# Kernel optimization log

Measured on AMD Instinct MI355X. Metric: run time of the kernel, lower is better.

Reference implementation:

```python
import jax, jax.numpy as jnp
import numpy as np

HIDDEN = 1024
HEADS = 16
B, L = 2, 2048


def _xavier(key, shape):
    fan_in, fan_out = shape[1], shape[0]
    limit = float(np.sqrt(6.0 / (fan_in + fan_out)))
    return jax.random.uniform(key, shape, jnp.float32, -limit, limit)


def setup_inputs() -> dict:
    key = jax.random.key(0)
    ks = jax.random.split(key, 6)
    return {
        "query": jax.random.normal(ks[0], (B, L, HIDDEN), jnp.float32),
        "bias": jax.random.normal(ks[1], (B, 1, 1, L), jnp.float32),
        "Wq": _xavier(ks[2], (HIDDEN, HIDDEN)), "bq": jnp.zeros((HIDDEN,), jnp.float32),
        "Wk": _xavier(ks[3], (HIDDEN, HIDDEN)), "bk": jnp.zeros((HIDDEN,), jnp.float32),
        "Wv": _xavier(ks[4], (HIDDEN, HIDDEN)), "bv": jnp.zeros((HIDDEN,), jnp.float32),
        "Wo": _xavier(ks[5], (HIDDEN, HIDDEN)), "bo": jnp.zeros((HIDDEN,), jnp.float32),
    }


def _split_heads(x):
    b, l, c = x.shape
    return x.reshape(b, l, HEADS, c // HEADS).transpose(0, 2, 1, 3)  # [B,H,L,d]


def reference(query, bias, Wq, bq, Wk, bk, Wv, bv, Wo, bo):
    d_head = HIDDEN // HEADS
    q = query @ Wq.T + bq
    k = query @ Wk.T + bk
    v = query @ Wv.T + bv
    q = _split_heads(q) * (d_head ** -0.5)  # [B,H,L,d]
    k = _split_heads(k)
    v = _split_heads(v)
    logits = jnp.einsum("bhqd,bhkd->bhqk", q, k) + bias  # [B,H,L,L]
    weights = jax.nn.softmax(logits, axis=-1)
    x = jnp.einsum("bhqk,bhkd->bhqd", weights, v)  # [B,H,L,d]
    x = x.transpose(0, 2, 1, 3).reshape(query.shape[0], query.shape[1], HIDDEN)
    return x @ Wo.T + bo
```

## Files before the change

kernel.cpp:

```cpp
#include <hip/hip_runtime.h>
#include <hip/hip_fp16.h>
#include <stdint.h>

#define HIDDEN 1024
#define HEADS  16
#define DH     64
#define B_     2
#define L_     2048
#define M_TOT  (B_ * L_)
#define ELEMS  (M_TOT * HIDDEN)
#define LOG2E  1.44269504088896340736f

typedef _Float16 f16;
typedef _Float16 f16x4 __attribute__((ext_vector_type(4)));
typedef _Float16 f16x8 __attribute__((ext_vector_type(8)));
typedef float    f32x4 __attribute__((ext_vector_type(4)));
typedef uint32_t u32;
typedef __attribute__((address_space(1))) u32 gu32;
typedef __attribute__((address_space(3))) u32 su32;

#define MFMA16(a, b, c) __builtin_amdgcn_mfma_f32_16x16x16f16(a, b, c, 0, 0, 0)
#define MFMA32(a, b, c) __builtin_amdgcn_mfma_f32_16x16x32_f16(a, b, c, 0, 0, 0)


__global__ __launch_bounds__(256)
void convert_f16(const float* __restrict__ query,
                 const float* __restrict__ Wq, const float* __restrict__ Wk,
                 const float* __restrict__ Wv, const float* __restrict__ Wo,
                 f16* __restrict__ Qh, f16* __restrict__ Wh)
{
    const int NQ4 = ELEMS / 4;
    const int NW4 = (HIDDEN * HIDDEN) / 4;
    const int total = NQ4 + 4 * NW4;
    for (int u = blockIdx.x * 256 + threadIdx.x; u < total; u += gridDim.x * 256) {
        float4 v; f16* dp;
        if (u < NQ4) {
            v = ((const float4*)query)[u];
            dp = Qh + (size_t)u * 4;
        } else {
            const int u2 = u - NQ4;
            const int w = u2 >> 18;
            const int off = u2 & (NW4 - 1);
            const float* W = (w == 0) ? Wq : (w == 1) ? Wk : (w == 2) ? Wv : Wo;
            v = ((const float4*)W)[off];
            dp = Wh + (size_t)u2 * 4;
        }
        f16x4 h = { (f16)v.x, (f16)v.y, (f16)v.z, (f16)v.w };
        *(f16x4*)dp = h;
    }
}

template<int TM, int TN>
__device__ __forceinline__
void gemm_loop(const f16* __restrict__ A, const f16* __restrict__ W,
               int mb, int nb, f32x4 (&acc)[TM / 32][TN / 32])
{
    __shared__ f16 As[TM * 32];
    __shared__ f16 Bs[TN * 32];

    const int tid  = threadIdx.x;
    const int lane = tid & 63;
    const int wave = tid >> 6;
    const int quad = lane >> 4;
    const int l16  = lane & 15;
    const int wm   = (wave >> 1) * (TM / 2);
    const int wn   = (wave & 1) * (TN / 2);

    constexpr int AISS = TM / 64;
    constexpr int BISS = TN / 64;
    int aoff[AISS], boff[BISS];
#pragma unroll
    for (int q = 0; q < AISS; q++) {
        const int p16 = (wave * AISS + q) * 64 + lane;
        const int r = p16 >> 2;
        const int c8 = (p16 & 3) ^ ((r >> 1) & 3);
        aoff[q] = (mb + r) * HIDDEN + c8 * 8;
    }
#pragma unroll
    for (int q = 0; q < BISS; q++) {
        const int p16 = (wave * BISS + q) * 64 + lane;
        const int r = p16 >> 2;
        const int c8 = (p16 & 3) ^ ((r >> 1) & 3);
        boff[q] = (nb + r) * HIDDEN + c8 * 8;
    }

    for (int kb = 0; kb < HIDDEN; kb += 32) {
#pragma unroll
        for (int q = 0; q < AISS; q++)
            __builtin_amdgcn_global_load_lds((gu32*)&A[aoff[q] + kb],
                                             (su32*)&As[(wave * AISS + q) * 512], 16, 0, 0);
#pragma unroll
        for (int q = 0; q < BISS; q++)
            __builtin_amdgcn_global_load_lds((gu32*)&W[boff[q] + kb],
                                             (su32*)&Bs[(wave * BISS + q) * 512], 16, 0, 0);
        __syncthreads();

        f16x8 af[TM / 32], bf[TN / 32];
#pragma unroll
        for (int i = 0; i < TM / 32; i++) {
            const int r = wm + i * 16 + l16;
            af[i] = *(const f16x8*)&As[r * 32 + (quad ^ ((r >> 1) & 3)) * 8];
        }
#pragma unroll
        for (int j = 0; j < TN / 32; j++) {
            const int r = wn + j * 16 + l16;
            bf[j] = *(const f16x8*)&Bs[r * 32 + (quad ^ ((r >> 1) & 3)) * 8];
        }
#pragma unroll
        for (int i = 0; i < TM / 32; i++)
#pragma unroll
            for (int j = 0; j < TN / 32; j++)
                acc[i][j] = MFMA32(af[i], bf[j], acc[i][j]);
        __syncthreads();
    }
}

__global__ __launch_bounds__(256)
void proj_qkv(const f16* __restrict__ A, const f16* __restrict__ W,
              const float* __restrict__ bq, const float* __restrict__ bk,
              const float* __restrict__ bv,
              f16* __restrict__ Qo, f16* __restrict__ Ko, f16* __restrict__ Vo)
{
    f32x4 acc[4][4] = {};
    const int mb = blockIdx.x * 128, nb = blockIdx.y * 128;
    gemm_loop<128, 128>(A, W, mb, nb, acc);

    const int lane = threadIdx.x & 63, wave = threadIdx.x >> 6;
    const int quad = lane >> 4, l16 = lane & 15;
    const int wm = (wave >> 1) * 64, wn = (wave & 1) * 64;
    const int nsel = nb >> 10;
    const int nbase = nb & 1023;

    if (nsel < 2) {
        const float* bias = nsel ? bk : bq;
        f16* out = nsel ? Ko : Qo;
        const float scale = nsel ? 1.0f : 0.125f * LOG2E;
#pragma unroll
        for (int i = 0; i < 4; i++)
#pragma unroll
            for (int j = 0; j < 4; j++) {
                const int n1 = nbase + wn + j * 16 + l16;
                const float bn = bias[n1];
                const int h = n1 >> 6, dd = n1 & 63;
#pragma unroll
                for (int r = 0; r < 4; r++) {
                    const int m = mb + wm + i * 16 + quad * 4 + r;
                    const int b = m >> 11, l = m & (L_ - 1);
                    out[(((b * HEADS + h) * L_) + l) * DH + dd] =
                        (f16)((acc[i][j][r] + bn) * scale);
                }
            }
    } else {
#pragma unroll
        for (int i = 0; i < 4; i++)
#pragma unroll
            for (int j = 0; j < 4; j++) {
                const int n1 = nbase + wn + j * 16 + l16;
                const float bn = bv[n1];
                const int h = n1 >> 6, dd = n1 & 63;
                const int m0 = mb + wm + i * 16 + quad * 4;
                const int b = m0 >> 11, l0 = m0 & (L_ - 1);
                f16x4 pk;
#pragma unroll
                for (int r = 0; r < 4; r++) pk[r] = (f16)(acc[i][j][r] + bn);
                *(f16x4*)&Vo[((size_t)(b * HEADS + h) * DH + dd) * L_ + l0] = pk;
            }
    }
}

__global__ __launch_bounds__(256)
void proj_out(const f16* __restrict__ A, const f16* __restrict__ W,
              const float* __restrict__ bo, float* __restrict__ out)
{
    f32x4 acc[4][2] = {};
    const int mb = blockIdx.x * 128, nb = blockIdx.y * 64;
    gemm_loop<128, 64>(A, W, mb, nb, acc);

    const int lane = threadIdx.x & 63, wave = threadIdx.x >> 6;
    const int quad = lane >> 4, l16 = lane & 15;
    const int wm = (wave >> 1) * 64, wn = (wave & 1) * 32;
#pragma unroll
    for (int i = 0; i < 4; i++)
#pragma unroll
        for (int j = 0; j < 2; j++) {
            const int n = nb + wn + j * 16 + l16;
            const float bn = bo[n];
#pragma unroll
            for (int r = 0; r < 4; r++) {
                const int m = mb + wm + i * 16 + quad * 4 + r;
                out[m * HIDDEN + n] = acc[i][j][r] + bn;
            }
        }
}

__global__ __launch_bounds__(256)
void attn(const f16* __restrict__ Q, const f16* __restrict__ K,
          const f16* __restrict__ Vt, const float* __restrict__ bias,
          f16* __restrict__ X)
{
    __shared__ f16 Ks[2][64 * 64];
    __shared__ f16 Vs[2][64 * 64];
    __shared__ float biasl[L_];

    const int tid  = threadIdx.x;
    const int lane = tid & 63;
    const int wave = tid >> 6;
    const int quad = lane >> 4;
    const int l16  = lane & 15;

    const int bh = blockIdx.x >> 4;
    const int b  = bh >> 4, h = bh & 15;
    const int qrow0 = (blockIdx.x & 15) * 128 + wave * 32;

    const f16* Qh  = Q  + (size_t)bh * L_ * DH;
    const f16* Kh  = K  + (size_t)bh * L_ * DH;
    const f16* Vth = Vt + (size_t)bh * DH * L_;

    {
        const float4* bb = (const float4*)(bias + b * L_);
        for (int i = tid; i < L_ / 4; i += 256) {
            const float4 v = bb[i];
            biasl[i * 4 + 0] = v.x * LOG2E;
            biasl[i * 4 + 1] = v.y * LOG2E;
            biasl[i * 4 + 2] = v.z * LOG2E;
            biasl[i * 4 + 3] = v.w * LOG2E;
        }
    }

    int krow[2], kcol[2];
#pragma unroll
    for (int q = 0; q < 2; q++) {
        const int grp = wave * 2 + q;
        const int r = grp * 8 + (lane >> 3);
        const int u = (lane & 7) ^ (r & 7);
        krow[q] = r; kcol[q] = u * 8;
    }

    f16x8 qf[2][2];
#pragma unroll
    for (int qt = 0; qt < 2; qt++)
#pragma unroll
        for (int hh = 0; hh < 2; hh++)
            qf[qt][hh] = *(const f16x8*)&Qh[(qrow0 + qt * 16 + l16) * DH + hh * 32 + quad * 8];

#pragma unroll
    for (int q = 0; q < 2; q++) {
        __builtin_amdgcn_global_load_lds((gu32*)(Kh + (size_t)krow[q] * DH + kcol[q]),
                                         (su32*)&Ks[0][(wave * 2 + q) * 512], 16, 0, 0);
        __builtin_amdgcn_global_load_lds((gu32*)(Vth + (size_t)krow[q] * L_ + kcol[q]),
                                         (su32*)&Vs[0][(wave * 2 + q) * 512], 16, 0, 0);
    }

    f32x4 o[2][4] = {};
    float lsum[2] = {};
    __syncthreads();

#pragma unroll 1
    for (int kb = 0; kb < L_; kb += 64) {
        const int buf = (kb >> 6) & 1;
        const int nkb = (kb + 64 < L_) ? kb + 64 : 0;

#pragma unroll
        for (int q = 0; q < 2; q++) {
            __builtin_amdgcn_global_load_lds(
                (gu32*)(Kh + (size_t)(nkb + krow[q]) * DH + kcol[q]),
                (su32*)&Ks[buf ^ 1][(wave * 2 + q) * 512], 16, 0, 0);
            __builtin_amdgcn_global_load_lds(
                (gu32*)(Vth + (size_t)krow[q] * L_ + nkb + kcol[q]),
                (su32*)&Vs[buf ^ 1][(wave * 2 + q) * 512], 16, 0, 0);
        }

#pragma unroll
        for (int c = 0; c < 4; c++) {
            const int krowc = c * 16 + l16;
            const f16x8 ka0 = *(const f16x8*)&Ks[buf][krowc * 64 + (quad ^ (krowc & 7)) * 8];
            const f16x8 ka1 = *(const f16x8*)&Ks[buf][krowc * 64 + ((quad + 4) ^ (krowc & 7)) * 8];
            f16x4 va[4];
#pragma unroll
            for (int t = 0; t < 4; t++) {
                const int vr = t * 16 + l16;
                const int uu = (c * 2 + (quad >> 1)) ^ (vr & 7);
                va[t] = *(const f16x4*)&Vs[buf][vr * 64 + uu * 8 + (quad & 1) * 4];
            }
            const f32x4 blv = *(const f32x4*)&biasl[kb + c * 16 + quad * 4];

#pragma unroll
            for (int qt = 0; qt < 2; qt++) {
                f32x4 z = { 0.f, 0.f, 0.f, 0.f };
                z = MFMA32(ka0, qf[qt][0], z);
                z = MFMA32(ka1, qf[qt][1], z);
                float p0 = __builtin_amdgcn_exp2f(z[0] + blv[0]);
                float p1 = __builtin_amdgcn_exp2f(z[1] + blv[1]);
                float p2 = __builtin_amdgcn_exp2f(z[2] + blv[2]);
                float p3 = __builtin_amdgcn_exp2f(z[3] + blv[3]);
                lsum[qt] += (p0 + p1) + (p2 + p3);
                const f16x4 pb = { (f16)p0, (f16)p1, (f16)p2, (f16)p3 };
#pragma unroll
                for (int t = 0; t < 4; t++)
                    o[qt][t] = MFMA16(va[t], pb, o[qt][t]);
            }
        }
        __syncthreads();
    }

#pragma unroll
    for (int qt = 0; qt < 2; qt++) {
        lsum[qt] += __shfl_xor(lsum[qt], 16);
        lsum[qt] += __shfl_xor(lsum[qt], 32);
    }

#pragma unroll
    for (int qt = 0; qt < 2; qt++) {
        const float inv = 1.0f / lsum[qt];
        const size_t qrow = (size_t)b * L_ + qrow0 + qt * 16 + l16;
#pragma unroll
        for (int t = 0; t < 4; t++) {
            f16x4 pk;
#pragma unroll
            for (int r = 0; r < 4; r++) pk[r] = (f16)(o[qt][t][r] * inv);
            *(f16x4*)&X[qrow * HIDDEN + h * DH + t * 16 + quad * 4] = pk;
        }
    }
}

extern "C" void kernel_launch(void* const* d_in, const int* in_sizes, int n_in,
                              void* d_out, int out_size, void* d_ws, size_t ws_size,
                              hipStream_t stream)
{
    const float* query = (const float*)d_in[0];
    const float* bias  = (const float*)d_in[1];
    const float* Wq = (const float*)d_in[2]; const float* bq = (const float*)d_in[3];
    const float* Wk = (const float*)d_in[4]; const float* bk = (const float*)d_in[5];
    const float* Wv = (const float*)d_in[6]; const float* bv = (const float*)d_in[7];
    const float* Wo = (const float*)d_in[8]; const float* bo = (const float*)d_in[9];
    float* out = (float*)d_out;

    f16* Wh = (f16*)d_ws;
    f16* Qh = Wh + 4096 * 1024;
    f16* Kf = Qh + ELEMS;
    f16* Vf = Kf + ELEMS;
    f16* Qf = Vf + ELEMS;
    f16* Xf = Qh;

    convert_f16<<<2048, 256, 0, stream>>>(query, Wq, Wk, Wv, Wo, Qh, Wh);
    proj_qkv<<<dim3(32, 24), 256, 0, stream>>>(Qh, Wh, bq, bk, bv, Qf, Kf, Vf);
    attn<<<512, 256, 0, stream>>>(Qf, Kf, Vf, bias, Xf);
    proj_out<<<dim3(32, 16), 256, 0, stream>>>(Xf, Wh + 3072 * 1024, bo, out);
}
```

Before: 222.6 us.

## Double-buffer GEMM LDS tiles and widen attention blocks to 512 threads

The shared GEMM loop now double-buffers its A/B LDS tiles, prefetching the next K-slice while MFMAs run on the current one, so global loads overlap with compute. The attention kernel moves to 512-thread blocks covering 256 query rows, which halves the number of times each K/V tile and the bias row are staged per head. Each thread now issues one K and one V async load per iteration instead of two. Trade-offs are double the GEMM LDS footprint and larger attention blocks, which may reduce occupancy. The GEMM loop appears to keep only one __syncthreads per iteration and drops the barrier after the load, which could risk a read/write race on the buffers.

New measurement: 382.5 us. +71.9%, slower.

```diff
diff --git a/kernel.cpp b/kernel.cpp
--- a/kernel.cpp
+++ b/kernel.cpp
@@ -55,8 +55,8 @@
 void gemm_loop(const f16* __restrict__ A, const f16* __restrict__ W,
                int mb, int nb, f32x4 (&acc)[TM / 32][TN / 32])
 {
-    __shared__ f16 As[TM * 32];
-    __shared__ f16 Bs[TN * 32];
+    __shared__ f16 As[2][TM * 32];
+    __shared__ f16 Bs[2][TN * 32];
 
     const int tid  = threadIdx.x;
     const int lane = tid & 63;
@@ -84,27 +84,39 @@
         boff[q] = (nb + r) * HIDDEN + c8 * 8;
     }
 
+#pragma unroll
+    for (int q = 0; q < AISS; q++)
+        __builtin_amdgcn_global_load_lds((gu32*)&A[aoff[q]],
+                                         (su32*)&As[0][(wave * AISS + q) * 512], 16, 0, 0);
+#pragma unroll
+    for (int q = 0; q < BISS; q++)
+        __builtin_amdgcn_global_load_lds((gu32*)&W[boff[q]],
+                                         (su32*)&Bs[0][(wave * BISS + q) * 512], 16, 0, 0);
+    __syncthreads();
+
     for (int kb = 0; kb < HIDDEN; kb += 32) {
+        const int buf = (kb >> 5) & 1;
+        const int nkb = (kb + 32 < HIDDEN) ? kb + 32 : 0;
+
 #pragma unroll
         for (int q = 0; q < AISS; q++)
-            __builtin_amdgcn_global_load_lds((gu32*)&A[aoff[q] + kb],
-                                             (su32*)&As[(wave * AISS + q) * 512], 16, 0, 0);
+            __builtin_amdgcn_global_load_lds((gu32*)&A[aoff[q] + nkb],
+                                             (su32*)&As[buf ^ 1][(wave * AISS + q) * 512], 16, 0, 0);
 #pragma unroll
         for (int q = 0; q < BISS; q++)
-            __builtin_amdgcn_global_load_lds((gu32*)&W[boff[q] + kb],
-                                             (su32*)&Bs[(wave * BISS + q) * 512], 16, 0, 0);
-        __syncthreads();
+            __builtin_amdgcn_global_load_lds((gu32*)&W[boff[q] + nkb],
+                                             (su32*)&Bs[buf ^ 1][(wave * BISS + q) * 512], 16, 0, 0);
 
         f16x8 af[TM / 32], bf[TN / 32];
 #pragma unroll
         for (int i = 0; i < TM / 32; i++) {
             const int r = wm + i * 16 + l16;
-            af[i] = *(const f16x8*)&As[r * 32 + (quad ^ ((r >> 1) & 3)) * 8];
+            af[i] = *(const f16x8*)&As[buf][r * 32 + (quad ^ ((r >> 1) & 3)) * 8];
         }
 #pragma unroll
         for (int j = 0; j < TN / 32; j++) {
             const int r = wn + j * 16 + l16;
-            bf[j] = *(const f16x8*)&Bs[r * 32 + (quad ^ ((r >> 1) & 3)) * 8];
+            bf[j] = *(const f16x8*)&Bs[buf][r * 32 + (quad ^ ((r >> 1) & 3)) * 8];
         }
 #pragma unroll
         for (int i = 0; i < TM / 32; i++)
@@ -193,7 +205,7 @@
         }
 }
 
-__global__ __launch_bounds__(256)
+__global__ __launch_bounds__(512, 6)
 void attn(const f16* __restrict__ Q, const f16* __restrict__ K,
           const f16* __restrict__ Vt, const float* __restrict__ bias,
           f16* __restrict__ X)
@@ -208,33 +220,24 @@
     const int quad = lane >> 4;
     const int l16  = lane & 15;
 
-    const int bh = blockIdx.x >> 4;
+    const int bh = blockIdx.x >> 3;
     const int b  = bh >> 4, h = bh & 15;
-    const int qrow0 = (blockIdx.x & 15) * 128 + wave * 32;
+    const int qrow0 = (blockIdx.x & 7) * 256 + wave * 32;
 
     const f16* Qh  = Q  + (size_t)bh * L_ * DH;
     const f16* Kh  = K  + (size_t)bh * L_ * DH;
     const f16* Vth = Vt + (size_t)bh * DH * L_;
 
     {
-        const float4* bb = (const float4*)(bias + b * L_);
-        for (int i = tid; i < L_ / 4; i += 256) {
-            const float4 v = bb[i];
-            biasl[i * 4 + 0] = v.x * LOG2E;
-            biasl[i * 4 + 1] = v.y * LOG2E;
-            biasl[i * 4 + 2] = v.z * LOG2E;
-            biasl[i * 4 + 3] = v.w * LOG2E;
-        }
-    }
-
-    int krow[2], kcol[2];
-#pragma unroll
-    for (int q = 0; q < 2; q++) {
-        const int grp = wave * 2 + q;
-        const int r = grp * 8 + (lane >> 3);
-        const int u = (lane & 7) ^ (r & 7);
-        krow[q] = r; kcol[q] = u * 8;
-    }
+        const float4 v = ((const float4*)(bias + b * L_))[tid];
+        biasl[tid * 4 + 0] = v.x * LOG2E;
+        biasl[tid * 4 + 1] = v.y * LOG2E;
+        biasl[tid * 4 + 2] = v.z * LOG2E;
+        biasl[tid * 4 + 3] = v.w * LOG2E;
+    }
+
+    const int srow = tid >> 3;
+    const int scol = ((tid & 7) ^ (srow & 7)) * 8;
 
     f16x8 qf[2][2];
 #pragma unroll
@@ -243,13 +246,10 @@
         for (int hh = 0; hh < 2; hh++)
             qf[qt][hh] = *(const f16x8*)&Qh[(qrow0 + qt * 16 + l16) * DH + hh * 32 + quad * 8];
 
-#pragma unroll
-    for (int q = 0; q < 2; q++) {
-        __builtin_amdgcn_global_load_lds((gu32*)(Kh + (size_t)krow[q] * DH + kcol[q]),
-                                         (su32*)&Ks[0][(wave * 2 + q) * 512], 16, 0, 0);
-        __builtin_amdgcn_global_load_lds((gu32*)(Vth + (size_t)krow[q] * L_ + kcol[q]),
-                                         (su32*)&Vs[0][(wave * 2 + q) * 512], 16, 0, 0);
-    }
+    __builtin_amdgcn_global_load_lds((gu32*)(Kh + (size_t)srow * DH + scol),
+                                     (su32*)&Ks[0][wave * 512], 16, 0, 0);
+    __builtin_amdgcn_global_load_lds((gu32*)(Vth + (size_t)srow * L_ + scol),
+                                     (su32*)&Vs[0][wave * 512], 16, 0, 0);
 
     f32x4 o[2][4] = {};
     float lsum[2] = {};
@@ -260,15 +260,10 @@
         const int buf = (kb >> 6) & 1;
         const int nkb = (kb + 64 < L_) ? kb + 64 : 0;
 
-#pragma unroll
-        for (int q = 0; q < 2; q++) {
-            __builtin_amdgcn_global_load_lds(
-                (gu32*)(Kh + (size_t)(nkb + krow[q]) * DH + kcol[q]),
-                (su32*)&Ks[buf ^ 1][(wave * 2 + q) * 512], 16, 0, 0);
-            __builtin_amdgcn_global_load_lds(
-                (gu32*)(Vth + (size_t)krow[q] * L_ + nkb + kcol[q]),
-                (su32*)&Vs[buf ^ 1][(wave * 2 + q) * 512], 16, 0, 0);
-        }
+        __builtin_amdgcn_global_load_lds((gu32*)(Kh + (size_t)(nkb + srow) * DH + scol),
+                                         (su32*)&Ks[buf ^ 1][wave * 512], 16, 0, 0);
+        __builtin_amdgcn_global_load_lds((gu32*)(Vth + (size_t)srow * L_ + nkb + scol),
+                                         (su32*)&Vs[buf ^ 1][wave * 512], 16, 0, 0);
 
 #pragma unroll
         for (int c = 0; c < 4; c++) {
@@ -344,6 +339,6 @@
 
     convert_f16<<<2048, 256, 0, stream>>>(query, Wq, Wk, Wv, Wo, Qh, Wh);
     proj_qkv<<<dim3(32, 24), 256, 0, stream>>>(Qh, Wh, bq, bk, bv, Qf, Kf, Vf);
-    attn<<<512, 256, 0, stream>>>(Qf, Kf, Vf, bias, Xf);
+    attn<<<256, 512, 0, stream>>>(Qf, Kf, Vf, bias, Xf);
     proj_out<<<dim3(32, 16), 256, 0, stream>>>(Xf, Wh + 3072 * 1024, bo, out);
 }
```

## Double-buffer GEMM LDS tiles and fold softmax bias and row-sum into MFMAs

Applied to the files above, without the earlier changes.

The projection GEMM loop now uses two LDS buffers, prefetching the next K-slice while computing on the current one, and drops one of the two barriers per iteration. In attention, the bias is fed in as the MFMA accumulator's initial value, so no separate adds are needed. The softmax row-sum is computed by an extra MFMA against a vector of ones, which replaces the scalar adds and the cross-lane shuffles. This doubles GEMM LDS usage, and the single remaining barrier must still cover the hazard between reading one buffer and overwriting the other. The row-sum is now accumulated from fp16-rounded probabilities, which slightly changes numerics.

After: 207.1 us. 7.0% less time.

```diff
diff --git a/kernel.cpp b/kernel.cpp
--- a/kernel.cpp
+++ b/kernel.cpp
@@ -55,8 +55,8 @@
 void gemm_loop(const f16* __restrict__ A, const f16* __restrict__ W,
                int mb, int nb, f32x4 (&acc)[TM / 32][TN / 32])
 {
-    __shared__ f16 As[TM * 32];
-    __shared__ f16 Bs[TN * 32];
+    __shared__ f16 As[2][TM * 32];
+    __shared__ f16 Bs[2][TN * 32];
 
     const int tid  = threadIdx.x;
     const int lane = tid & 63;
@@ -84,27 +84,39 @@
         boff[q] = (nb + r) * HIDDEN + c8 * 8;
     }
 
+#pragma unroll
+    for (int q = 0; q < AISS; q++)
+        __builtin_amdgcn_global_load_lds((gu32*)&A[aoff[q]],
+                                         (su32*)&As[0][(wave * AISS + q) * 512], 16, 0, 0);
+#pragma unroll
+    for (int q = 0; q < BISS; q++)
+        __builtin_amdgcn_global_load_lds((gu32*)&W[boff[q]],
+                                         (su32*)&Bs[0][(wave * BISS + q) * 512], 16, 0, 0);
+    __syncthreads();
+
     for (int kb = 0; kb < HIDDEN; kb += 32) {
+        const int buf = (kb >> 5) & 1;
+        const int nkb = (kb + 32 < HIDDEN) ? kb + 32 : 0;
+
 #pragma unroll
         for (int q = 0; q < AISS; q++)
-            __builtin_amdgcn_global_load_lds((gu32*)&A[aoff[q] + kb],
-                                             (su32*)&As[(wave * AISS + q) * 512], 16, 0, 0);
+            __builtin_amdgcn_global_load_lds((gu32*)&A[aoff[q] + nkb],
+                                             (su32*)&As[buf ^ 1][(wave * AISS + q) * 512], 16, 0, 0);
 #pragma unroll
         for (int q = 0; q < BISS; q++)
-            __builtin_amdgcn_global_load_lds((gu32*)&W[boff[q] + kb],
-                                             (su32*)&Bs[(wave * BISS + q) * 512], 16, 0, 0);
-        __syncthreads();
+            __builtin_amdgcn_global_load_lds((gu32*)&W[boff[q] + nkb],
+                                             (su32*)&Bs[buf ^ 1][(wave * BISS + q) * 512], 16, 0, 0);
 
         f16x8 af[TM / 32], bf[TN / 32];
 #pragma unroll
         for (int i = 0; i < TM / 32; i++) {
             const int r = wm + i * 16 + l16;
-            af[i] = *(const f16x8*)&As[r * 32 + (quad ^ ((r >> 1) & 3)) * 8];
+            af[i] = *(const f16x8*)&As[buf][r * 32 + (quad ^ ((r >> 1) & 3)) * 8];
         }
 #pragma unroll
         for (int j = 0; j < TN / 32; j++) {
             const int r = wn + j * 16 + l16;
-            bf[j] = *(const f16x8*)&Bs[r * 32 + (quad ^ ((r >> 1) & 3)) * 8];
+            bf[j] = *(const f16x8*)&Bs[buf][r * 32 + (quad ^ ((r >> 1) & 3)) * 8];
         }
 #pragma unroll
         for (int i = 0; i < TM / 32; i++)
@@ -252,7 +264,8 @@
     }
 
     f32x4 o[2][4] = {};
-    float lsum[2] = {};
+    f32x4 osum[2] = {};
+    const f16x4 ones = { (f16)1.f, (f16)1.f, (f16)1.f, (f16)1.f };
     __syncthreads();
 
 #pragma unroll 1
@@ -286,18 +299,17 @@
 
 #pragma unroll
             for (int qt = 0; qt < 2; qt++) {
-                f32x4 z = { 0.f, 0.f, 0.f, 0.f };
+                f32x4 z = blv;
                 z = MFMA32(ka0, qf[qt][0], z);
                 z = MFMA32(ka1, qf[qt][1], z);
-                float p0 = __builtin_amdgcn_exp2f(z[0] + blv[0]);
-                float p1 = __builtin_amdgcn_exp2f(z[1] + blv[1]);
-                float p2 = __builtin_amdgcn_exp2f(z[2] + blv[2]);
-                float p3 = __builtin_amdgcn_exp2f(z[3] + blv[3]);
-                lsum[qt] += (p0 + p1) + (p2 + p3);
-                const f16x4 pb = { (f16)p0, (f16)p1, (f16)p2, (f16)p3 };
+                const f16x4 pb = { (f16)__builtin_amdgcn_exp2f(z[0]),
+                                   (f16)__builtin_amdgcn_exp2f(z[1]),
+                                   (f16)__builtin_amdgcn_exp2f(z[2]),
+                                   (f16)__builtin_amdgcn_exp2f(z[3]) };
 #pragma unroll
                 for (int t = 0; t < 4; t++)
                     o[qt][t] = MFMA16(va[t], pb, o[qt][t]);
+                osum[qt] = MFMA16(ones, pb, osum[qt]);
             }
         }
         __syncthreads();
@@ -305,13 +317,7 @@
 
 #pragma unroll
     for (int qt = 0; qt < 2; qt++) {
-        lsum[qt] += __shfl_xor(lsum[qt], 16);
-        lsum[qt] += __shfl_xor(lsum[qt], 32);
-    }
-
-#pragma unroll
-    for (int qt = 0; qt < 2; qt++) {
-        const float inv = 1.0f / lsum[qt];
+        const float inv = 1.0f / osum[qt][0];
         const size_t qrow = (size_t)b * L_ + qrow0 + qt * 16 + l16;
 #pragma unroll
         for (int t = 0; t < 4; t++) {
```
